# Kernel tuning notes

Hardware: AMD Instinct MI355X
Metric: run time of the kernel (lower is better)

Reference implementation:

```python
import jax, jax.numpy as jnp
import numpy as np

IN_DIM = 128
NUM_KERNELS = 512
OUT_DIM = 256
EPS_NORM = 1e-09


def setup_inputs() -> dict:
    key = jax.random.key(0)
    k1, k2, k3, k4 = jax.random.split(key, 4)
    inp = jax.random.normal(k1, (16, 512, IN_DIM), dtype=jnp.float32)
    # centers ~ U[-1, 1] as in reset(upper_bound_kernels=1.0)
    centers = jax.random.uniform(k2, (NUM_KERNELS, IN_DIM), dtype=jnp.float32, minval=-1.0, maxval=1.0)
    # log shapes ~ N(0, 0.1)
    log_shapes = 0.1 * jax.random.normal(k3, (NUM_KERNELS,), dtype=jnp.float32)
    # xavier-uniform weights, gain=1: bound = sqrt(6/(fan_in+fan_out))
    bound = float(np.sqrt(6.0 / (NUM_KERNELS + OUT_DIM)))
    weights = jax.random.uniform(k4, (OUT_DIM, NUM_KERNELS), dtype=jnp.float32, minval=-bound, maxval=bound)
    return {"input": inp, "kernels_centers": centers, "log_shapes": log_shapes, "weights": weights}


def reference(input, kernels_centers, log_shapes, weights):
    lead = input.shape[:-1]
    x = input.reshape(-1, input.shape[-1])            # (N, D)
    diff = x[:, None, :] - kernels_centers[None, :, :]  # (N, K, D)
    r = jnp.linalg.norm(diff, axis=-1)                 # (N, K)
    eps_r = jnp.exp(log_shapes)[None, :] * r           # (N, K)
    rbfs = jnp.exp(-eps_r ** 2)                        # gaussian RBF
    rbfs = rbfs / (jnp.sum(rbfs, axis=-1, keepdims=True) + EPS_NORM)
    out = rbfs @ weights.T                             # (N, OUT)
    return out.reshape(lead + (weights.shape[0],))
```

## Files before the change

### kernel.cpp

```cpp
#include <hip/hip_runtime.h>

typedef float  f32x4 __attribute__((ext_vector_type(4)));
typedef short  s16x8 __attribute__((ext_vector_type(8)));
typedef ushort u16x8 __attribute__((ext_vector_type(8)));

constexpr int D  = 128;
constexpr int K  = 512;
constexpr int O  = 256;
constexpr int NT = 256;
constexpr float NL2E = -1.44269504088896340736f;

__device__ __forceinline__ ushort f2bf(float f) {
    uint u = __builtin_bit_cast(uint, f);
    return (ushort)((u + 0x7FFFu + ((u >> 16) & 1u)) >> 16);
}
__device__ __forceinline__ float bf2f(ushort h) {
    return __builtin_bit_cast(float, ((uint)h) << 16);
}

__global__ __launch_bounds__(NT)
void rbf_prep(const float* __restrict__ x, const float* __restrict__ cen,
              const float* __restrict__ ls, const float* __restrict__ w,
              ushort* __restrict__ Xh, ushort* __restrict__ Xl,
              ushort* __restrict__ Ch, ushort* __restrict__ Cl,
              ushort* __restrict__ Wf, float* __restrict__ xs2,
              float2* __restrict__ ecs, int nxb, int ncb)
{
    __shared__ float red[4][16];
    const int b = blockIdx.x, t = threadIdx.x, lane = t & 63, wq = t >> 6;

    if (b < nxb + ncb) {
        const bool isX  = b < nxb;
        const int panel = isX ? b : (b - nxb);
        const float* src = isX ? x : cen;
        ushort* dh = isX ? Xh : Ch;
        ushort* dl = isX ? Xl : Cl;
        const int row = panel * 16 + (lane & 15);
        const int col = wq * 32 + (lane >> 4) * 8;
        const float* p = src + (size_t)row * D + col;
        float4 v0 = *(const float4*)p, v1 = *(const float4*)(p + 4);
        float f[8] = {v0.x, v0.y, v0.z, v0.w, v1.x, v1.y, v1.z, v1.w};
        u16x8 h, l;
        float s = 0.f;
#pragma unroll
        for (int j = 0; j < 8; ++j) {
            s = fmaf(f[j], f[j], s);
            ushort hb = f2bf(f[j]);
            h[j] = hb;
            l[j] = f2bf(f[j] - bf2f(hb));
        }
        const size_t c = ((size_t)panel * 4 + wq) * 64 + lane;
        *(u16x8*)&dh[c * 8] = h;
        *(u16x8*)&dl[c * 8] = l;
        s += __shfl_xor(s, 16);
        s += __shfl_xor(s, 32);
        if (lane < 16) red[wq][lane] = s;
        __syncthreads();
        if (t < 16) {
            float sum = red[0][t] + red[1][t] + red[2][t] + red[3][t];
            if (isX) {
                xs2[panel * 16 + t] = sum;
            } else {
                int k = panel * 16 + t;
                float e = __expf(2.0f * ls[k]);
                ecs[k] = make_float2(NL2E * e, NL2E * e * sum);
            }
        }
    } else {
        const int c0 = (b - nxb - ncb) * NT + t;
        const int ln = c0 & 63, ot = (c0 >> 6) & 15, ks = c0 >> 10;
        const int o  = ot * 16 + (ln & 15);
        const int kb = ks * 32 + (ln >> 4) * 8;
        const float* p = w + (size_t)o * K + kb;
        float4 v0 = *(const float4*)p, v1 = *(const float4*)(p + 4);
        u16x8 h;
        h[0] = f2bf(v0.x); h[1] = f2bf(v0.y); h[2] = f2bf(v0.z); h[3] = f2bf(v0.w);
        h[4] = f2bf(v1.x); h[5] = f2bf(v1.y); h[6] = f2bf(v1.z); h[7] = f2bf(v1.w);
        *(u16x8*)&Wf[(size_t)c0 * 8] = h;
    }
}

constexpr int PP = 40;

__global__ __launch_bounds__(NT, 2)
void rbf_main(const ushort* __restrict__ Xh, const ushort* __restrict__ Xl,
              const ushort* __restrict__ Ch, const ushort* __restrict__ Cl,
              const ushort* __restrict__ Wf, const float* __restrict__ xs2,
              const float2* __restrict__ ecs, float* __restrict__ out)
{
    __shared__ ushort Ps[2][4][16][PP];
    __shared__ float  Acc[2][16][O + 4];
    __shared__ float  Ls[4][16];

    const int t = threadIdx.x, lane = t & 63, wv = t >> 6;
    const int l15 = lane & 15, l4 = lane >> 4;
    const int nb = blockIdx.x * 16;

    s16x8 xh[4], xl[4];
    {
        const size_t base = ((size_t)blockIdx.x * 4) * 64 + lane;
#pragma unroll
        for (int q = 0; q < 4; ++q) {
            xh[q] = *(const s16x8*)&Xh[(base + q * 64) * 8];
            xl[q] = *(const s16x8*)&Xl[(base + q * 64) * 8];
        }
    }
    const float xs2v = xs2[nb + l15];

    f32x4 oacc[16];
#pragma unroll
    for (int i = 0; i < 16; ++i) oacc[i] = (f32x4){0.f, 0.f, 0.f, 0.f};
    float Lp = 0.f;

    s16x8 ch[2][2][4], cl[2][2][4];
#define LOADC(buf, s_) {                                                    \
    _Pragma("unroll") for (int bt = 0; bt < 2; ++bt) {                      \
        const size_t kt = (size_t)(wv * 8 + (s_) * 2 + bt);                 \
        _Pragma("unroll") for (int q = 0; q < 4; ++q) {                     \
            const size_t cc = ((kt * 4 + q) * 64 + lane) * 8;               \
            ch[buf][bt][q] = *(const s16x8*)&Ch[cc];                        \
            cl[buf][bt][q] = *(const s16x8*)&Cl[cc];                        \
        } } }

    LOADC(0, 0);

#pragma unroll
    for (int s = 0; s < 4; ++s) {
        const int cur = s & 1, nxt = cur ^ 1;
        const ushort* wbase = &Wf[((((size_t)(wv * 4 + s)) * 16) * 64 + lane) * 8];

        if (s < 3) LOADC(nxt, s + 1);

#pragma unroll
        for (int bt = 0; bt < 2; ++bt) {
            f32x4 ghh = (f32x4){0.f,0.f,0.f,0.f};
            f32x4 ghl = (f32x4){0.f,0.f,0.f,0.f};
            f32x4 glh = (f32x4){0.f,0.f,0.f,0.f};
#pragma unroll
            for (int q = 0; q < 4; ++q) {
                ghh = __builtin_amdgcn_mfma_f32_16x16x32_bf16(ch[cur][bt][q], xh[q], ghh, 0, 0, 0);
                ghl = __builtin_amdgcn_mfma_f32_16x16x32_bf16(ch[cur][bt][q], xl[q], ghl, 0, 0, 0);
                glh = __builtin_amdgcn_mfma_f32_16x16x32_bf16(cl[cur][bt][q], xh[q], glh, 0, 0, 0);
            }
            f32x4 g = ghh + ghl + glh;

            const int kbase = wv * 128 + s * 32 + bt * 16 + l4 * 4;
            float4 e0 = *(const float4*)&ecs[kbase];
            float4 e1 = *(const float4*)&ecs[kbase + 2];
            float ph0 = exp2f(fmaf(e0.x, fmaf(-2.f, g[0], xs2v), e0.y));
            float ph1 = exp2f(fmaf(e0.z, fmaf(-2.f, g[1], xs2v), e0.w));
            float ph2 = exp2f(fmaf(e1.x, fmaf(-2.f, g[2], xs2v), e1.y));
            float ph3 = exp2f(fmaf(e1.z, fmaf(-2.f, g[3], xs2v), e1.w));
            Lp += (ph0 + ph1) + (ph2 + ph3);
            uint p0 = (uint)f2bf(ph0) | ((uint)f2bf(ph1) << 16);
            uint p1 = (uint)f2bf(ph2) | ((uint)f2bf(ph3) << 16);
            *(uint2*)&Ps[cur][wv][l15][bt * 16 + l4 * 4] = make_uint2(p0, p1);
        }

        s16x8 pa = *(const s16x8*)&Ps[cur][wv][l15][l4 * 8];
#pragma unroll
        for (int ot = 0; ot < 16; ++ot) {
            s16x8 bfr = *(const s16x8*)&wbase[(size_t)ot * 64 * 8];
            oacc[ot] = __builtin_amdgcn_mfma_f32_16x16x32_bf16(pa, bfr, oacc[ot], 0, 0, 0);
        }
    }
#undef LOADC

    {
        float v = Lp;
        v += __shfl_xor(v, 16);
        v += __shfl_xor(v, 32);
        if (lane < 16) Ls[wv][lane] = v;
    }

    if (wv < 2) {
#pragma unroll
        for (int ot = 0; ot < 16; ++ot)
#pragma unroll
            for (int r = 0; r < 4; ++r)
                Acc[wv][l4 * 4 + r][ot * 16 + l15] = oacc[ot][r];
    }
    __syncthreads();
    if (wv >= 2) {
#pragma unroll
        for (int ot = 0; ot < 16; ++ot)
#pragma unroll
            for (int r = 0; r < 4; ++r)
                Acc[wv - 2][l4 * 4 + r][ot * 16 + l15] += oacc[ot][r];
    }
    __syncthreads();

#pragma unroll
    for (int rr = 0; rr < 4; ++rr) {
        const int n = wv * 4 + rr;
        float inv = 1.0f / (Ls[0][n] + Ls[1][n] + Ls[2][n] + Ls[3][n] + 1e-9f);
        float4 a0 = *(const float4*)&Acc[0][n][lane * 4];
        float4 a1 = *(const float4*)&Acc[1][n][lane * 4];
        float4 o4;
        o4.x = (a0.x + a1.x) * inv;
        o4.y = (a0.y + a1.y) * inv;
        o4.z = (a0.z + a1.z) * inv;
        o4.w = (a0.w + a1.w) * inv;
        *(float4*)&out[(size_t)(nb + n) * O + lane * 4] = o4;
    }
}

__global__ __launch_bounds__(NT, 2)
void rbf_fb(const float* __restrict__ x, const float* __restrict__ cen,
            const float* __restrict__ ls, const float* __restrict__ w,
            float* __restrict__ out)
{
    __shared__ ushort Ps[2][4][16][PP];
    __shared__ float  Acc[2][16][O + 4];
    __shared__ float  Ls[4][16];
    const int t = threadIdx.x, lane = t & 63, wv = t >> 6;
    const int l15 = lane & 15, l4 = lane >> 4;
    const int nb = blockIdx.x * 16;

    s16x8 xh[4], xl[4];
    float sx = 0.f;
    {
        const float* xr = x + (size_t)(nb + l15) * D;
#pragma unroll
        for (int q = 0; q < 4; ++q) {
            float4 v0 = *(const float4*)(xr + q * 32 + l4 * 8);
            float4 v1 = *(const float4*)(xr + q * 32 + l4 * 8 + 4);
            float f[8] = {v0.x, v0.y, v0.z, v0.w, v1.x, v1.y, v1.z, v1.w};
            s16x8 h, lo;
#pragma unroll
            for (int j = 0; j < 8; ++j) {
                sx = fmaf(f[j], f[j], sx);
                ushort hb = f2bf(f[j]);
                h[j] = (short)hb; lo[j] = (short)f2bf(f[j] - bf2f(hb));
            }
            xh[q] = h; xl[q] = lo;
        }
    }
    sx += __shfl_xor(sx, 16); sx += __shfl_xor(sx, 32);
    float xs2v[4];
#pragma unroll
    for (int r = 0; r < 4; ++r) xs2v[r] = __shfl(sx, l4 * 4 + r);

    f32x4 oacc[16];
#pragma unroll
    for (int ot = 0; ot < 16; ++ot) oacc[ot] = (f32x4){0.f,0.f,0.f,0.f};
    float Lp[4] = {0.f,0.f,0.f,0.f};
    const int kq = wv * (K / 4);

#pragma unroll
    for (int s = 0; s < 4; ++s) {
        const int k0 = kq + s * 32;
#pragma unroll
        for (int bt = 0; bt < 2; ++bt) {
            const int kk = k0 + bt * 16 + l15;
            const float* cr = cen + (size_t)kk * D;
            s16x8 ch[4], cl[4];
            float sc = 0.f;
#pragma unroll
            for (int q = 0; q < 4; ++q) {
                float4 v0 = *(const float4*)(cr + q * 32 + l4 * 8);
                float4 v1 = *(const float4*)(cr + q * 32 + l4 * 8 + 4);
                float f[8] = {v0.x, v0.y, v0.z, v0.w, v1.x, v1.y, v1.z, v1.w};
                s16x8 h, lo;
#pragma unroll
                for (int j = 0; j < 8; ++j) {
                    sc = fmaf(f[j], f[j], sc);
                    ushort hb = f2bf(f[j]);
                    h[j] = (short)hb; lo[j] = (short)f2bf(f[j] - bf2f(hb));
                }
                ch[q] = h; cl[q] = lo;
            }
            sc += __shfl_xor(sc, 16); sc += __shfl_xor(sc, 32);
            float es_ = __expf(2.0f * ls[kk]);
            f32x4 ghh={0,0,0,0}, ghl={0,0,0,0}, glh={0,0,0,0};
#pragma unroll
            for (int q = 0; q < 4; ++q) {
                ghh = __builtin_amdgcn_mfma_f32_16x16x32_bf16(xh[q], ch[q], ghh, 0,0,0);
                ghl = __builtin_amdgcn_mfma_f32_16x16x32_bf16(xh[q], cl[q], ghl, 0,0,0);
                glh = __builtin_amdgcn_mfma_f32_16x16x32_bf16(xl[q], ch[q], glh, 0,0,0);
            }
            f32x4 gg = ghh + ghl + glh;
#pragma unroll
            for (int r = 0; r < 4; ++r) {
                float r2 = xs2v[r] + sc - 2.0f * gg[r];
                float ph = __expf(-es_ * r2);
                Lp[r] += ph;
                Ps[s & 1][wv][l4 * 4 + r][bt * 16 + l15] = f2bf(ph);
            }
        }
        s16x8 pa = *(const s16x8*)&Ps[s & 1][wv][l15][l4 * 8];
#pragma unroll
        for (int ot = 0; ot < 16; ++ot) {
            const float* wr = w + (size_t)(ot * 16 + l15) * K + k0;
            float4 v0 = *(const float4*)(wr + l4 * 8);
            float4 v1 = *(const float4*)(wr + l4 * 8 + 4);
            s16x8 b;
            b[0]=(short)f2bf(v0.x); b[1]=(short)f2bf(v0.y); b[2]=(short)f2bf(v0.z); b[3]=(short)f2bf(v0.w);
            b[4]=(short)f2bf(v1.x); b[5]=(short)f2bf(v1.y); b[6]=(short)f2bf(v1.z); b[7]=(short)f2bf(v1.w);
            oacc[ot] = __builtin_amdgcn_mfma_f32_16x16x32_bf16(pa, b, oacc[ot], 0,0,0);
        }
    }
#pragma unroll
    for (int r = 0; r < 4; ++r) {
        float v = Lp[r];
        v += __shfl_xor(v, 1); v += __shfl_xor(v, 2);
        v += __shfl_xor(v, 4); v += __shfl_xor(v, 8);
        if (l15 == 0) Ls[wv][l4 * 4 + r] = v;
    }
    if (wv < 2) {
#pragma unroll
        for (int ot = 0; ot < 16; ++ot)
#pragma unroll
            for (int r = 0; r < 4; ++r)
                Acc[wv][l4 * 4 + r][ot * 16 + l15] = oacc[ot][r];
    }
    __syncthreads();
    if (wv >= 2) {
#pragma unroll
        for (int ot = 0; ot < 16; ++ot)
#pragma unroll
            for (int r = 0; r < 4; ++r)
                Acc[wv - 2][l4 * 4 + r][ot * 16 + l15] += oacc[ot][r];
    }
    __syncthreads();
#pragma unroll
    for (int rr = 0; rr < 4; ++rr) {
        const int n = wv * 4 + rr;
        float inv = 1.0f / (Ls[0][n] + Ls[1][n] + Ls[2][n] + Ls[3][n] + 1e-9f);
        float4 a0 = *(const float4*)&Acc[0][n][lane * 4];
        float4 a1 = *(const float4*)&Acc[1][n][lane * 4];
        float4 o4;
        o4.x = (a0.x + a1.x) * inv; o4.y = (a0.y + a1.y) * inv;
        o4.z = (a0.z + a1.z) * inv; o4.w = (a0.w + a1.w) * inv;
        *(float4*)&out[(size_t)(nb + n) * O + lane * 4] = o4;
    }
}

extern "C" void kernel_launch(void* const* d_in, const int* in_sizes, int n_in,
                              void* d_out, int out_size, void* d_ws, size_t ws_size,
                              hipStream_t stream) {
    const float* x   = (const float*)d_in[0];
    const float* cen = (const float*)d_in[1];
    const float* ls  = (const float*)d_in[2];
    const float* w   = (const float*)d_in[3];
    float* out = (float*)d_out;
    const int N = in_sizes[0] / D;

    size_t oXh = 0;
    size_t oXl = oXh + (size_t)N * D * 2;
    size_t oCh = oXl + (size_t)N * D * 2;
    size_t oCl = oCh + (size_t)K * D * 2;
    size_t oWf = oCl + (size_t)K * D * 2;
    size_t oxs = oWf + (size_t)O * K * 2;
    size_t oec = oxs + (size_t)N * 4;
    size_t need = oec + (size_t)K * 8;

    if (ws_size < need || (N % 16) != 0) {
        dim3 grid(N / 16), block(NT);
        hipLaunchKernelGGL(rbf_fb, grid, block, 0, stream, x, cen, ls, w, out);
        return;
    }

    char* ws = (char*)d_ws;
    ushort* Xh = (ushort*)(ws + oXh);
    ushort* Xl = (ushort*)(ws + oXl);
    ushort* Ch = (ushort*)(ws + oCh);
    ushort* Cl = (ushort*)(ws + oCl);
    ushort* Wf = (ushort*)(ws + oWf);
    float*  xs2 = (float*)(ws + oxs);
    float2* ecs = (float2*)(ws + oec);

    const int nxb = N / 16;
    const int ncb = K / 16;
    const int nwb = (O * K / 8) / NT;
    dim3 pgrid(nxb + ncb + nwb), pblock(NT);
    hipLaunchKernelGGL(rbf_prep, pgrid, pblock, 0, stream,
                       x, cen, ls, w, Xh, Xl, Ch, Cl, Wf, xs2, ecs, nxb, ncb);

    dim3 grid(N / 16), block(NT);
    hipLaunchKernelGGL(rbf_main, grid, block, 0, stream,
                       Xh, Xl, Ch, Cl, Wf, xs2, ecs, out);
}
```

Baseline: 27.72 us.

## Split K reduction across eight waves per block with staggered LDS accumulation

The main kernel now runs 512 threads (8 waves) per 16-row block, so each wave covers 64 RBF centers instead of 128, with no double-buffered center prefetch. Per-wave output partials are reduced into a single LDS accumulator over 8 staggered rounds, each wave touching a different output slice per round and separated by barriers. The goal is more parallelism and latency hiding per block. In exchange it adds more barriers and LDS read-modify-write traffic, and occupancy depends on register pressure under the new launch bounds.

```diff
diff --git a/kernel.cpp b/kernel.cpp
--- a/kernel.cpp
+++ b/kernel.cpp
@@ -82,15 +82,15 @@
 
 constexpr int PP = 40;
 
-__global__ __launch_bounds__(NT, 2)
+__global__ __launch_bounds__(512, 4)
 void rbf_main(const ushort* __restrict__ Xh, const ushort* __restrict__ Xl,
               const ushort* __restrict__ Ch, const ushort* __restrict__ Cl,
               const ushort* __restrict__ Wf, const float* __restrict__ xs2,
               const float2* __restrict__ ecs, float* __restrict__ out)
 {
-    __shared__ ushort Ps[2][4][16][PP];
-    __shared__ float  Acc[2][16][O + 4];
-    __shared__ float  Ls[4][16];
+    __shared__ ushort Ps[8][16][PP];
+    __shared__ float  Acc[16][O + 4];
+    __shared__ float  Ls[8][16];
 
     const int t = threadIdx.x, lane = t & 63, wv = t >> 6;
     const int l15 = lane & 15, l4 = lane >> 4;
@@ -112,39 +112,32 @@
     for (int i = 0; i < 16; ++i) oacc[i] = (f32x4){0.f, 0.f, 0.f, 0.f};
     float Lp = 0.f;
 
-    s16x8 ch[2][2][4], cl[2][2][4];
-#define LOADC(buf, s_) {                                                    \
-    _Pragma("unroll") for (int bt = 0; bt < 2; ++bt) {                      \
-        const size_t kt = (size_t)(wv * 8 + (s_) * 2 + bt);                 \
-        _Pragma("unroll") for (int q = 0; q < 4; ++q) {                     \
-            const size_t cc = ((kt * 4 + q) * 64 + lane) * 8;               \
-            ch[buf][bt][q] = *(const s16x8*)&Ch[cc];                        \
-            cl[buf][bt][q] = *(const s16x8*)&Cl[cc];                        \
-        } } }
-
-    LOADC(0, 0);
-
-#pragma unroll
-    for (int s = 0; s < 4; ++s) {
-        const int cur = s & 1, nxt = cur ^ 1;
-        const ushort* wbase = &Wf[((((size_t)(wv * 4 + s)) * 16) * 64 + lane) * 8];
-
-        if (s < 3) LOADC(nxt, s + 1);
+#pragma unroll
+    for (int s = 0; s < 2; ++s) {
+        const ushort* wbase = &Wf[((((size_t)(wv * 2 + s)) * 16) * 64 + lane) * 8];
 
 #pragma unroll
         for (int bt = 0; bt < 2; ++bt) {
+            const size_t kt16 = (size_t)(wv * 4 + s * 2 + bt);
+            s16x8 ch[4], cl[4];
+#pragma unroll
+            for (int q = 0; q < 4; ++q) {
+                const size_t cc = ((kt16 * 4 + q) * 64 + lane) * 8;
+                ch[q] = *(const s16x8*)&Ch[cc];
+                cl[q] = *(const s16x8*)&Cl[cc];
+            }
             f32x4 ghh = (f32x4){0.f,0.f,0.f,0.f};
             f32x4 ghl = (f32x4){0.f,0.f,0.f,0.f};
             f32x4 glh = (f32x4){0.f,0.f,0.f,0.f};
 #pragma unroll
             for (int q = 0; q < 4; ++q) {
-                ghh = __builtin_amdgcn_mfma_f32_16x16x32_bf16(ch[cur][bt][q], xh[q], ghh, 0, 0, 0);
-                ghl = __builtin_amdgcn_mfma_f32_16x16x32_bf16(ch[cur][bt][q], xl[q], ghl, 0, 0, 0);
-                glh = __builtin_amdgcn_mfma_f32_16x16x32_bf16(cl[cur][bt][q], xh[q], glh, 0, 0, 0);
+                ghh = __builtin_amdgcn_mfma_f32_16x16x32_bf16(ch[q], xh[q], ghh, 0, 0, 0);
+                ghl = __builtin_amdgcn_mfma_f32_16x16x32_bf16(ch[q], xl[q], ghl, 0, 0, 0);
+                glh = __builtin_amdgcn_mfma_f32_16x16x32_bf16(cl[q], xh[q], glh, 0, 0, 0);
             }
             f32x4 g = ghh + ghl + glh;
 
-            const int kbase = wv * 128 + s * 32 + bt * 16 + l4 * 4;
+            const int kbase = wv * 64 + s * 32 + bt * 16 + l4 * 4;
             float4 e0 = *(const float4*)&ecs[kbase];
             float4 e1 = *(const float4*)&ecs[kbase + 2];
             float ph0 = exp2f(fmaf(e0.x, fmaf(-2.f, g[0], xs2v), e0.y));
@@ -154,17 +147,16 @@
             Lp += (ph0 + ph1) + (ph2 + ph3);
             uint p0 = (uint)f2bf(ph0) | ((uint)f2bf(ph1) << 16);
             uint p1 = (uint)f2bf(ph2) | ((uint)f2bf(ph3) << 16);
-            *(uint2*)&Ps[cur][wv][l15][bt * 16 + l4 * 4] = make_uint2(p0, p1);
-        }
-
-        s16x8 pa = *(const s16x8*)&Ps[cur][wv][l15][l4 * 8];
+            *(uint2*)&Ps[wv][l15][bt * 16 + l4 * 4] = make_uint2(p0, p1);
+        }
+
+        s16x8 pa = *(const s16x8*)&Ps[wv][l15][l4 * 8];
 #pragma unroll
         for (int ot = 0; ot < 16; ++ot) {
             s16x8 bfr = *(const s16x8*)&wbase[(size_t)ot * 64 * 8];
             oacc[ot] = __builtin_amdgcn_mfma_f32_16x16x32_bf16(pa, bfr, oacc[ot], 0, 0, 0);
         }
     }
-#undef LOADC
 
     {
         float v = Lp;
@@ -173,35 +165,42 @@
         if (lane < 16) Ls[wv][lane] = v;
     }
 
-    if (wv < 2) {
-#pragma unroll
-        for (int ot = 0; ot < 16; ++ot)
-#pragma unroll
-            for (int r = 0; r < 4; ++r)
-                Acc[wv][l4 * 4 + r][ot * 16 + l15] = oacc[ot][r];
-    }
-    __syncthreads();
-    if (wv >= 2) {
-#pragma unroll
-        for (int ot = 0; ot < 16; ++ot)
-#pragma unroll
-            for (int r = 0; r < 4; ++r)
-                Acc[wv - 2][l4 * 4 + r][ot * 16 + l15] += oacc[ot][r];
-    }
-    __syncthreads();
-
-#pragma unroll
-    for (int rr = 0; rr < 4; ++rr) {
-        const int n = wv * 4 + rr;
-        float inv = 1.0f / (Ls[0][n] + Ls[1][n] + Ls[2][n] + Ls[3][n] + 1e-9f);
-        float4 a0 = *(const float4*)&Acc[0][n][lane * 4];
-        float4 a1 = *(const float4*)&Acc[1][n][lane * 4];
-        float4 o4;
-        o4.x = (a0.x + a1.x) * inv;
-        o4.y = (a0.y + a1.y) * inv;
-        o4.z = (a0.z + a1.z) * inv;
-        o4.w = (a0.w + a1.w) * inv;
-        *(float4*)&out[(size_t)(nb + n) * O + lane * 4] = o4;
+#pragma unroll
+    for (int st = 0; st < 8; ++st) {
+        const int oq = (wv + st) & 7;
+        if (st == 0) {
+#pragma unroll
+            for (int j = 0; j < 2; ++j) {
+                const int ot = oq * 2 + j;
+#pragma unroll
+                for (int r = 0; r < 4; ++r)
+                    Acc[l4 * 4 + r][ot * 16 + l15] = oacc[ot][r];
+            }
+        } else {
+#pragma unroll
+            for (int j = 0; j < 2; ++j) {
+                const int ot = oq * 2 + j;
+#pragma unroll
+                for (int r = 0; r < 4; ++r)
+                    Acc[l4 * 4 + r][ot * 16 + l15] += oacc[ot][r];
+            }
+        }
+        __syncthreads();
+    }
+
+    {
+        const int n  = t >> 5;
+        const int c8 = (t & 31) * 8;
+        float inv = 1.0f / (Ls[0][n] + Ls[1][n] + Ls[2][n] + Ls[3][n] +
+                            Ls[4][n] + Ls[5][n] + Ls[6][n] + Ls[7][n] + 1e-9f);
+        float4 a0 = *(const float4*)&Acc[n][c8];
+        float4 a1 = *(const float4*)&Acc[n][c8 + 4];
+        float4 o0, o1;
+        o0.x = a0.x * inv; o0.y = a0.y * inv; o0.z = a0.z * inv; o0.w = a0.w * inv;
+        o1.x = a1.x * inv; o1.y = a1.y * inv; o1.z = a1.z * inv; o1.w = a1.w * inv;
+        float* po = &out[(size_t)(nb + n) * O + c8];
+        *(float4*)po = o0;
+        *(float4*)(po + 4) = o1;
     }
 }
 
@@ -210,9 +209,9 @@
             const float* __restrict__ ls, const float* __restrict__ w,
             float* __restrict__ out)
 {
-    __shared__ ushort Ps[2][4][16][PP];
-    __shared__ float  Acc[2][16][O + 4];
-    __shared__ float  Ls[4][16];
+    __shared__ ushort Ps2[2][4][16][PP];
+    __shared__ float  Acc2[2][16][O + 4];
+    __shared__ float  Ls2[4][16];
     const int t = threadIdx.x, lane = t & 63, wv = t >> 6;
     const int l15 = lane & 15, l4 = lane >> 4;
     const int nb = blockIdx.x * 16;
@@ -285,10 +284,10 @@
                 float r2 = xs2v[r] + sc - 2.0f * gg[r];
                 float ph = __expf(-es_ * r2);
                 Lp[r] += ph;
-                Ps[s & 1][wv][l4 * 4 + r][bt * 16 + l15] = f2bf(ph);
-            }
-        }
-        s16x8 pa = *(const s16x8*)&Ps[s & 1][wv][l15][l4 * 8];
+                Ps2[s & 1][wv][l4 * 4 + r][bt * 16 + l15] = f2bf(ph);
+            }
+        }
+        s16x8 pa = *(const s16x8*)&Ps2[s & 1][wv][l15][l4 * 8];
 #pragma unroll
         for (int ot = 0; ot < 16; ++ot) {
             const float* wr = w + (size_t)(ot * 16 + l15) * K + k0;
@@ -305,14 +304,14 @@
         float v = Lp[r];
         v += __shfl_xor(v, 1); v += __shfl_xor(v, 2);
         v += __shfl_xor(v, 4); v += __shfl_xor(v, 8);
-        if (l15 == 0) Ls[wv][l4 * 4 + r] = v;
+        if (l15 == 0) Ls2[wv][l4 * 4 + r] = v;
     }
     if (wv < 2) {
 #pragma unroll
         for (int ot = 0; ot < 16; ++ot)
 #pragma unroll
             for (int r = 0; r < 4; ++r)
-                Acc[wv][l4 * 4 + r][ot * 16 + l15] = oacc[ot][r];
+                Acc2[wv][l4 * 4 + r][ot * 16 + l15] = oacc[ot][r];
     }
     __syncthreads();
     if (wv >= 2) {
@@ -320,15 +319,15 @@
         for (int ot = 0; ot < 16; ++ot)
 #pragma unroll
             for (int r = 0; r < 4; ++r)
-                Acc[wv - 2][l4 * 4 + r][ot * 16 + l15] += oacc[ot][r];
+                Acc2[wv - 2][l4 * 4 + r][ot * 16 + l15] += oacc[ot][r];
     }
     __syncthreads();
 #pragma unroll
     for (int rr = 0; rr < 4; ++rr) {
         const int n = wv * 4 + rr;
-        float inv = 1.0f / (Ls[0][n] + Ls[1][n] + Ls[2][n] + Ls[3][n] + 1e-9f);
-        float4 a0 = *(const float4*)&Acc[0][n][lane * 4];
-        float4 a1 = *(const float4*)&Acc[1][n][lane * 4];
+        float inv = 1.0f / (Ls2[0][n] + Ls2[1][n] + Ls2[2][n] + Ls2[3][n] + 1e-9f);
+        float4 a0 = *(const float4*)&Acc2[0][n][lane * 4];
+        float4 a1 = *(const float4*)&Acc2[1][n][lane * 4];
         float4 o4;
         o4.x = (a0.x + a1.x) * inv; o4.y = (a0.y + a1.y) * inv;
         o4.z = (a0.z + a1.z) * inv; o4.w = (a0.w + a1.w) * inv;
@@ -377,7 +376,7 @@
     hipLaunchKernelGGL(rbf_prep, pgrid, pblock, 0, stream,
                        x, cen, ls, w, Xh, Xl, Ch, Cl, Wf, xs2, ecs, nxb, ncb);
 
-    dim3 grid(N / 16), block(NT);
+    dim3 grid(N / 16), block(512);
     hipLaunchKernelGGL(rbf_main, grid, block, 0, stream,
                        Xh, Xl, Ch, Cl, Wf, xs2, ecs, out);
 }
```

Measured after the change: 43.71 us. 57.7% more time.
